# Kernel tuning notes

Measured on AMD Instinct MI355X. Metric: run time of the kernel, lower is better.

The kernel has to match this reference:

```python
import jax, jax.numpy as jnp
import numpy as np

EPS = 1e-12  # torch F.normalize eps

def _l2norm(t, axis):
    n = jnp.linalg.norm(t, axis=axis, keepdims=True)
    return t / jnp.maximum(n, EPS)

def setup_inputs() -> dict:
    key = jax.random.key(0)
    ks = jax.random.split(key, 7)
    B, L, D, F, K = 16, 128, 512, 1024, 16
    return {
        "x": jax.random.normal(ks[0], (B, L, D), jnp.float32),
        "W_gate_basis": jax.random.normal(ks[1], (K, D, F), jnp.float32) * (1.0 / np.sqrt(D)),
        "W_up_basis": jax.random.normal(ks[2], (K, D, F), jnp.float32) * (1.0 / np.sqrt(D)),
        "W_down_basis": jax.random.normal(ks[3], (K, F, D), jnp.float32) * (1.0 / np.sqrt(F)),
        "token_coef1": jax.random.normal(ks[4], (L, K), jnp.float32),
        "token_coef2": jax.random.normal(ks[5], (L, K), jnp.float32),
        "token_coef3": jax.random.normal(ks[6], (L, K), jnp.float32),
        "u_scale_param": jnp.ones((1, F), jnp.float32),
        "v_scale_param": jnp.ones((1, F), jnp.float32),
    }

def reference(x, W_gate_basis, W_up_basis, W_down_basis,
              token_coef1, token_coef2, token_coef3,
              u_scale_param, v_scale_param):
    D = x.shape[-1]
    c1 = jax.nn.softmax(token_coef1, axis=-1)
    c2 = jax.nn.softmax(token_coef2, axis=-1)
    c3 = jax.nn.softmax(token_coef3, axis=-1)
    # per-token weights [L, D, F] / [L, F, D]
    W_gate = jnp.einsum('lk,kio->lio', c1, W_gate_basis)
    W_up = jnp.einsum('lk,kio->lio', c2, W_up_basis)
    W_down = jnp.einsum('lk,koj->loj', c3, W_down_basis)
    W_gate = _l2norm(W_gate, axis=1)   # normalize over input dim D
    W_up = _l2norm(W_up, axis=1)
    W_down = _l2norm(W_down, axis=1)   # normalize over hidden dim F
    u = jnp.einsum('bld,ldf->blf', x, W_gate)
    v = jnp.einsum('bld,ldf->blf', x, W_up)
    u_scale = jnp.abs(u_scale_param) * 1.0
    v_scale = jnp.abs(v_scale_param) * jnp.sqrt(jnp.float32(D))
    h = jax.nn.silu(v_scale * v) * (u_scale * u)
    out = jnp.einsum('blf,lfd->bld', h, W_down)
    return _l2norm(out, axis=-1)
```

## Files before the change

kernel.cpp:

```cpp
#include <hip/hip_runtime.h>
#include <hip/hip_bf16.h>
#include <cmath>


typedef _Float16 half8 __attribute__((ext_vector_type(8)));
typedef _Float16 half4 __attribute__((ext_vector_type(4)));
typedef float    f32x4 __attribute__((ext_vector_type(4)));
typedef float    f32x2 __attribute__((ext_vector_type(2)));

#define MFMA_F16  __builtin_amdgcn_mfma_f32_16x16x32_f16
#define MFMA16    __builtin_amdgcn_mfma_f32_16x16x16f16

#define LDS_BARRIER()                                           \
    do {                                                        \
        asm volatile("s_waitcnt lgkmcnt(0)" ::: "memory");      \
        __builtin_amdgcn_s_barrier();                           \
    } while (0)

static constexpr size_t OFF_P1  = 0;
static constexpr size_t OFF_P2  = 16777216;
static constexpr size_t OFF_P3n = 17825792;
static constexpr size_t OFF_XA  = 33554432;
static constexpr size_t OFF_U2  = 35651584;
static constexpr size_t OFF_S   = 39845888;
// ... 22 lines not shown
#pragma unroll
    for (int k = 0; k < 16; ++k) {
        f32x4 v = *(const f32x4*)(
            src + (size_t)k * Amin * Bmaj + (size_t)(m0 + row) * Bmaj + M0 + cg * 4);
        f32x2 lo = { v[0], v[1] };
        f32x2 hi = { v[2], v[3] };
        *(f32x2*)(&S[k * 1088 + row * 34 + cg * 4])     = lo;
        *(f32x2*)(&S[k * 1088 + row * 34 + cg * 4 + 2]) = hi;
    }
    __syncthreads();

    int mn = t & 31, mjq = t >> 5;
#pragma unroll
    for (int q = 0; q < 4; ++q) {
        int mj = q * 8 + mjq;
        half8 v0, v1;
#pragma unroll
        for (int k = 0; k < 8; ++k) v0[k] = (_Float16)S[k * 1088 + mn * 34 + mj];
#pragma unroll
        for (int k = 0; k < 8; ++k) v1[k] = (_Float16)S[(k + 8) * 1088 + mn * 34 + mj];
        _Float16* out = dst + ((size_t)(M0 + mj) * Amin + m0 + mn) * 16;
        *(half8*)out       = v0;
        *(half8*)(out + 8) = v1;
    }
}

__global__ __launch_bounds__(256) void prep_x(
    const float* __restrict__ x, _Float16* __restrict__ XA)
{
    int l = blockIdx.x >> 1, bh = blockIdx.x & 1;
    __shared__ __align__(16) _Float16 XT[8][524];
    int t = threadIdx.x;

    int bl = t >> 5, q = t & 31;
    int b = bh * 8 + bl;
#pragma unroll
    for (int j = 0; j < 4; ++j) {
        f32x4 v = *(const f32x4*)(x + ((size_t)(b * 128 + l) * 512 + j * 128 + q * 4));
#pragma unroll
        for (int i = 0; i < 4; ++i)
            XT[bl][j * 128 + q * 4 + i] = (_Float16)v[i];
    }
    __syncthreads();

    int c = t >> 2, bi = t & 3;
#pragma unroll
    for (int s = 0; s < 2; ++s) {
        int blw = bi * 2 + s;
        half8 h = *(const half8*)(&XT[blw][c * 8]);
        *(half8*)(XA + (((size_t)(l * 64 + c) * 16 + bh * 8 + blw) * 8)) = h;
    }
}

__global__ __launch_bounds__(256, 4) void up_split(
    const _Float16* __restrict__ P1, const _Float16* __restrict__ P2,
    const _Float16* __restrict__ XA,
    const float* __restrict__ tc1, const float* __restrict__ tc2,
    const float* __restrict__ usp, const float* __restrict__ vsp,
    _Float16* __restrict__ U2, _Float16* __restrict__ S)
{
    int bid = blockIdx.x;
    int mh = bid >> 9;
    int lg = (bid >> 6) & 7;
    int f0 = (bid & 63) * 16;
    int tid = threadIdx.x;
    int w = tid >> 6, lane = tid & 63;
    int n = lane & 15, kc = lane >> 4;

    const _Float16* P  = mh ? P2 : P1;
    const float*    tc = mh ? tc2 : tc1;

    __shared__ __align__(16) _Float16 Wt[2][16 * 584];
    __shared__ float CN[256];

    const _Float16* pP  = P + ((size_t)(f0 + w * 4) * 512 + n) * 16 + kc * 4;
    const _Float16* pXA = XA + (((size_t)(lg * 16 + w * 4) * 64 + kc) * 16 + n) * 8;

    half4 pa[4][2];
#pragma unroll
    for (int fl = 0; fl < 4; ++fl)
#pragma unroll
        for (int dg = 0; dg < 2; ++dg)
            pa[fl][dg] = *(const half4*)(pP + fl * 8192 + dg * 256);
    const _Float16* qP = pP + 512;

    if (tid < 16) {
        const float* row = tc + (size_t)(lg * 16 + tid) * 16;
        float e[16], m = -1e30f, sum = 0.f;
#pragma unroll
        for (int k = 0; k < 16; ++k) m = fmaxf(m, row[k]);
#pragma unroll
        for (int k = 0; k < 16; ++k) { e[k] = __expf(row[k] - m); sum += e[k]; }
        float r = 1.f / sum;
#pragma unroll
        for (int k = 0; k < 16; ++k) CN[tid * 16 + k] = e[k] * r;
    }
    __syncthreads();

    half4 cf;
#pragma unroll
    for (int j = 0; j < 4; ++j)
        cf[j] = (_Float16)CN[n * 16 + kc * 4 + j];

    f32x4 zf = { 0.f, 0.f, 0.f, 0.f };
    f32x4 aU[4];
#pragma unroll
    for (int i = 0; i < 4; ++i) aU[i] = zf;
    float nsq[4] = { 0.f, 0.f, 0.f, 0.f };
    half8 xf[4];

#pragma unroll 1
    for (int it = 0; it < 16; ++it) {
        _Float16* WtW = &Wt[it & 1][0];
        const _Float16* WtR = &Wt[(it & 1) ^ 1][0];

#pragma unroll
        for (int fl = 0; fl < 4; ++fl) {
            int f_l = w * 4 + fl;
#pragma unroll
            for (int dg = 0; dg < 2; ++dg) {
                f32x4 c1 = MFMA16(pa[fl][dg], cf, zf, 0, 0, 0);
                nsq[fl] += c1[0] * c1[0] + c1[1] * c1[1]
                         + c1[2] * c1[2] + c1[3] * c1[3];
                half4 h1 = { (_Float16)c1[0], (_Float16)c1[1],
                             (_Float16)c1[2], (_Float16)c1[3] };
                *(half4*)(&WtW[n * 584 + f_l * 36 + dg * 16 + kc * 4]) = h1;
            }
        }
        if (it < 15) {
#pragma unroll
            for (int fl = 0; fl < 4; ++fl)
#pragma unroll
                for (int dg = 0; dg < 2; ++dg)
                    pa[fl][dg] = *(const half4*)(qP + fl * 8192 + dg * 256);
        }
        if (it > 0) {
#pragma unroll
            for (int li = 0; li < 4; ++li) {
                int l = w * 4 + li;
                half8 wU = *(const half8*)(&WtR[l * 584 + n * 36 + kc * 8]);
                aU[li] = MFMA_F16(xf[li], wU, aU[li], 0, 0, 0);
            }
        }
#pragma unroll
        for (int li = 0; li < 4; ++li)
            xf[li] = *(const half8*)(pXA + li * 8192);
        pXA += 512;
        qP += 512;
        LDS_BARRIER();
    }
#pragma unroll
    for (int li = 0; li < 4; ++li) {
        int l = w * 4 + li;
        half8 wU = *(const half8*)(&Wt[1][l * 584 + n * 36 + kc * 8]);
        aU[li] = MFMA_F16(xf[li], wU, aU[li], 0, 0, 0);
    }

#pragma unroll
    for (int fl = 0; fl < 4; ++fl) {
        float vU = nsq[fl];
        vU += __shfl_xor(vU, 16); vU += __shfl_xor(vU, 32);
        if (kc == 0) CN[n * 16 + w * 4 + fl] = vU;
    }
    __syncthreads();

    int f = f0 + n;
    float sc = mh ? (fabsf(vsp[f]) * 22.627416997969522f)
                  : fabsf(usp[f]);
    _Float16* Out = mh ? S : U2;
#pragma unroll
    for (int li = 0; li < 4; ++li) {
        int lgl = lg * 16 + w * 4 + li;
        float r1 = 1.f / fmaxf(sqrtf(CN[(w * 4 + li) * 16 + n]), 1e-12f);
#pragma unroll
        for (int i = 0; i < 4; ++i) {
            float val = aU[li][i] * r1 * sc;
            if (mh) val = val / (1.f + __expf(-val));
            Out[(((size_t)lgl * 128 + (f >> 3)) * 16 + kc * 4 + i) * 8 + (f & 7)] =
                (_Float16)val;
        }
    }
}

__global__ __launch_bounds__(256, 4) void down_fast(
    const _Float16* __restrict__ P3, const float* __restrict__ tc3,
    const _Float16* __restrict__ S, const _Float16* __restrict__ U2,
    float* __restrict__ Rp, float* __restrict__ Np)
{
    int zh = blockIdx.x >> 8;
    int rem = blockIdx.x & 255;
    int lg = rem >> 5;
    int d0 = (rem & 31) * 16;
    int tid = threadIdx.x;
    int w = tid >> 6, lane = tid & 63;
    int n = lane & 15, kc = lane >> 4;

    __shared__ __align__(16) _Float16 Wt[2][16 * 584];
    __shared__ float CN[256];

    const _Float16* pP3 = P3 + ((size_t)(d0 + w * 4) * 1024 + zh * 256 + n) * 16 + kc * 4;
    size_t hoff = (((size_t)(lg * 16 + w * 4) * 128 + zh * 32 + kc) * 16 + n) * 8;
    const _Float16* pS = S + hoff;
    const _Float16* pU = U2 + hoff;

    half4 pa[4][2];
#pragma unroll
    for (int dl = 0; dl < 4; ++dl)
#pragma unroll
        for (int fg = 0; fg < 2; ++fg)
            pa[dl][fg] = *(const half4*)(pP3 + dl * 16384 + fg * 256);
    const _Float16* qP3 = pP3 + 512;

    if (tid < 16) {
        const float* row = tc3 + (size_t)(lg * 16 + tid) * 16;
        float e[16], m = -1e30f, sum = 0.f;
#pragma unroll
        for (int k = 0; k < 16; ++k) m = fmaxf(m, row[k]);
#pragma unroll
        for (int k = 0; k < 16; ++k) { e[k] = __expf(row[k] - m); sum += e[k]; }
        float r = 1.f / sum;
#pragma unroll
        for (int k = 0; k < 16; ++k) CN[tid * 16 + k] = e[k] * r;
    }
    __syncthreads();

    half4 cf3;
#pragma unroll
    for (int j = 0; j < 4; ++j)
        cf3[j] = (_Float16)CN[n * 16 + kc * 4 + j];

    f32x4 zf = { 0.f, 0.f, 0.f, 0.f };
    f32x4 aO[4];
#pragma unroll
    for (int i = 0; i < 4; ++i) aO[i] = zf;
    float nsqD[4] = { 0.f, 0.f, 0.f, 0.f };
    half8 hf[4];

#pragma unroll 1
    for (int it = 0; it < 8; ++it) {
        _Float16* WtW = &Wt[it & 1][0];
        const _Float16* WtR = &Wt[(it & 1) ^ 1][0];

#pragma unroll
        for (int dl = 0; dl < 4; ++dl) {
            int d_l = w * 4 + dl;
#pragma unroll
            for (int fg = 0; fg < 2; ++fg) {
                f32x4 cw = MFMA16(pa[dl][fg], cf3, zf, 0, 0, 0);
                nsqD[dl] += cw[0] * cw[0] + cw[1] * cw[1]
                          + cw[2] * cw[2] + cw[3] * cw[3];
                half4 h4 = { (_Float16)cw[0], (_Float16)cw[1],
                             (_Float16)cw[2], (_Float16)cw[3] };
                *(half4*)(&WtW[n * 584 + d_l * 36 + fg * 16 + kc * 4]) = h4;
            }
        }
        if (it < 7) {
#pragma unroll
            for (int dl = 0; dl < 4; ++dl)
#pragma unroll
                for (int fg = 0; fg < 2; ++fg)
                    pa[dl][fg] = *(const half4*)(qP3 + dl * 16384 + fg * 256);
        }
        if (it > 0) {
#pragma unroll
            for (int li = 0; li < 4; ++li) {
                int l = w * 4 + li;
                half8 wf = *(const half8*)(&WtR[l * 584 + n * 36 + kc * 8]);
                aO[li] = MFMA_F16(hf[li], wf, aO[li], 0, 0, 0);
            }
        }
#pragma unroll
        for (int li = 0; li < 4; ++li) {
            half8 s8 = *(const half8*)(pS + li * 16384);
            half8 u8 = *(const half8*)(pU + li * 16384);
            hf[li] = s8 * u8;
        }
        pS += 512;
        pU += 512;
        qP3 += 512;
        LDS_BARRIER();
    }
#pragma unroll
    for (int li = 0; li < 4; ++li) {
        int l = w * 4 + li;
        half8 wf = *(const half8*)(&Wt[1][l * 584 + n * 36 + kc * 8]);
        aO[li] = MFMA_F16(hf[li], wf, aO[li], 0, 0, 0);
    }

#pragma unroll
    for (int dl = 0; dl < 4; ++dl) {
        float v = nsqD[dl];
        v += __shfl_xor(v, 16); v += __shfl_xor(v, 32);
        if (kc == 0)
            Np[(size_t)zh * 65536 + (size_t)(lg * 16 + n) * 512 + d0 + w * 4 + dl] = v;
    }
#pragma unroll
    for (int li = 0; li < 4; ++li) {
        int lgl = lg * 16 + w * 4 + li;
#pragma unroll
        for (int i = 0; i < 4; ++i)
            Rp[(size_t)zh * 1048576 +
               ((size_t)(kc * 4 + i) * 128 + lgl) * 512 + d0 + n] = aO[li][i];
    }
}

__global__ __launch_bounds__(128) void final_combine(
    const float* __restrict__ Rp, const float* __restrict__ Np,
    float* __restrict__ out)
{
    int rid = blockIdx.x;
    int l = rid & 127;
    int t = threadIdx.x;
    f32x4 r = { 0.f, 0.f, 0.f, 0.f };
    f32x4 nn = { 0.f, 0.f, 0.f, 0.f };
#pragma unroll
    for (int zh = 0; zh < 4; ++zh) {
        f32x4 rz = *(const f32x4*)(Rp + (size_t)zh * 1048576 + (size_t)rid * 512 + t * 4);
        f32x4 nz = *(const f32x4*)(Np + (size_t)zh * 65536 + (size_t)l * 512 + t * 4);
#pragma unroll
        for (int j = 0; j < 4; ++j) { r[j] += rz[j]; nn[j] += nz[j]; }
    }
    f32x4 y;
#pragma unroll
    for (int j = 0; j < 4; ++j) {
        float rr = 1.f / fmaxf(sqrtf(fmaxf(nn[j], 0.f)), 1e-12f);
        y[j] = r[j] * rr;
    }
    float s = y[0] * y[0] + y[1] * y[1] + y[2] * y[2] + y[3] * y[3];
#pragma unroll
    for (int off = 32; off > 0; off >>= 1) s += __shfl_down(s, off);
    __shared__ float sred[2];
    if ((t & 63) == 0) sred[t >> 6] = s;
    __syncthreads();
    float rr = 1.f / fmaxf(sqrtf(sred[0] + sred[1]), 1e-12f);
    f32x4 o = { y[0] * rr, y[1] * rr, y[2] * rr, y[3] * rr };
    *(f32x4*)(out + (size_t)rid * 512 + t * 4) = o;
}

__global__ __launch_bounds__(256) void up_kernel(
    const float* __restrict__ x,
    const float* __restrict__ wg, const float* __restrict__ wu,
    const float* __restrict__ tc1, const float* __restrict__ tc2,
    const float* __restrict__ usp, const float* __restrict__ vsp,
    _Float16* __restrict__ Hp)
{
    int lg = blockIdx.x >> 6;
    int f0 = (blockIdx.x & 63) * 16;
    int tid = threadIdx.x;
    int w = tid >> 6, lane = tid & 63;
    int n = lane & 15, kc = lane >> 4;

    __shared__ __align__(16) _Float16 Xt[256 * 40];
    __shared__ __align__(16) _Float16 Bh[32 * 16 * 24];
    __shared__ __align__(16) _Float16 Wt[16 * 528];
    __shared__ float CN[2 * 16 * 16];
// ... 250 lines not shown
        int lgl = lg * 16 + w * 4 + li;
        float r3 = 1.f / fmaxf(sqrtf(CN[(w * 4 + li) * 16 + n]), 1e-12f);
#pragma unroll
        for (int i = 0; i < 4; ++i)
            out[((size_t)(kc * 4 + i) * 128 + lgl) * 512 + d0 + n] = aO[li][i] * r3;
    }
}

__global__ __launch_bounds__(128) void final_kernel(float* __restrict__ out)
{
    int rid = blockIdx.x;
    int t = threadIdx.x;
    f32x4 y = *(const f32x4*)(out + (size_t)rid * 512 + t * 4);
    float s = y[0] * y[0] + y[1] * y[1] + y[2] * y[2] + y[3] * y[3];
#pragma unroll
    for (int off = 32; off > 0; off >>= 1) s += __shfl_down(s, off);
    __shared__ float sred[2];
    if ((t & 63) == 0) sred[t >> 6] = s;
    __syncthreads();
    float rr = 1.f / fmaxf(sqrtf(sred[0] + sred[1]), 1e-12f);
    f32x4 o = { y[0] * rr, y[1] * rr, y[2] * rr, y[3] * rr };
    *(f32x4*)(out + (size_t)rid * 512 + t * 4) = o;
}

extern "C" void kernel_launch(void* const* d_in, const int* in_sizes, int n_in,
                              void* d_out, int out_size, void* d_ws, size_t ws_size,
                              hipStream_t stream)
{
    (void)in_sizes; (void)n_in; (void)out_size;
    const float* x   = (const float*)d_in[0];
    const float* wg  = (const float*)d_in[1];
    const float* wu  = (const float*)d_in[2];
    const float* wd  = (const float*)d_in[3];
    const float* tc1 = (const float*)d_in[4];
    const float* tc2 = (const float*)d_in[5];
    const float* tc3 = (const float*)d_in[6];
    const float* usp = (const float*)d_in[7];
    const float* vsp = (const float*)d_in[8];
    float* outp = (float*)d_out;
    char* ws = (char*)d_ws;

    if (ws_size >= WS_FAST) {
        _Float16* P1  = (_Float16*)(ws + OFF_P1);
        _Float16* P2  = (_Float16*)(ws + OFF_P2);
        _Float16* P3n = (_Float16*)(ws + OFF_P3n);
        _Float16* XA  = (_Float16*)(ws + OFF_XA);
        _Float16* U2  = (_Float16*)(ws + OFF_U2);
        _Float16* S   = (_Float16*)(ws + OFF_S);
        float* Rp = (float*)(ws + OFF_P1);
        float* Np = (float*)(ws + OFF_P2);
        prep_basis_all<<<dim3(512, 2), dim3(256), 0, stream>>>(
            wg, wu, wd, P1, P2, P3n, 0);
        prep_x<<<dim3(256), dim3(256), 0, stream>>>(x, XA);
        up_split<<<dim3(1024), dim3(256), 0, stream>>>(P1, P2, XA, tc1, tc2,
                                                       usp, vsp, U2, S);
        prep_basis_all<<<dim3(512, 1), dim3(256), 0, stream>>>(
            wg, wu, wd, P1, P2, P3n, 2);
        down_fast<<<dim3(1024), dim3(256), 0, stream>>>(P3n, tc3, S, U2, Rp, Np);
        final_combine<<<dim3(2048), dim3(128), 0, stream>>>(Rp, Np, outp);
    } else {
        _Float16* Hp = (_Float16*)ws;
        up_kernel<<<dim3(512), dim3(256), 0, stream>>>(x, wg, wu, tc1, tc2,
                                                       usp, vsp, Hp);
        down_kernel<<<dim3(256), dim3(256), 0, stream>>>(wd, tc3, Hp, outp);
        final_kernel<<<dim3(2048), dim3(128), 0, stream>>>(outp);
    }
}
```

Before: 227.1 us.

## Unroll main loops by two with even/odd register sets for deeper prefetch

```diff
diff --git a/kernel.cpp b/kernel.cpp
--- a/kernel.cpp
+++ b/kernel.cpp
@@ -118,17 +118,26 @@
 
     __shared__ __align__(16) _Float16 Wt[2][16 * 584];
     __shared__ float CN[256];
+    _Float16* Wt0 = &Wt[0][0];
+    _Float16* Wt1 = &Wt[1][0];
 
     const _Float16* pP  = P + ((size_t)(f0 + w * 4) * 512 + n) * 16 + kc * 4;
     const _Float16* pXA = XA + (((size_t)(lg * 16 + w * 4) * 64 + kc) * 16 + n) * 8;
 
-    half4 pa[4][2];
+    half4 paE[4][2], paO[4][2];
+    half8 xfE[4], xfO[4];
 #pragma unroll
     for (int fl = 0; fl < 4; ++fl)
 #pragma unroll
-        for (int dg = 0; dg < 2; ++dg)
-            pa[fl][dg] = *(const half4*)(pP + fl * 8192 + dg * 256);
-    const _Float16* qP = pP + 512;
+        for (int dg = 0; dg < 2; ++dg) {
+            paE[fl][dg] = *(const half4*)(pP + fl * 8192 + dg * 256);
+            paO[fl][dg] = *(const half4*)(pP + 512 + fl * 8192 + dg * 256);
+        }
+#pragma unroll
+    for (int li = 0; li < 4; ++li)
+        xfE[li] = *(const half8*)(pXA + li * 8192);
+    const _Float16* qP  = pP + 1024;
+    const _Float16* qXA = pXA + 512;
 
     if (tid < 16) {
         const float* row = tc + (size_t)(lg * 16 + tid) * 16;
@@ -153,53 +162,120 @@
 #pragma unroll
     for (int i = 0; i < 4; ++i) aU[i] = zf;
     float nsq[4] = { 0.f, 0.f, 0.f, 0.f };
-    half8 xf[4];
 
 #pragma unroll 1
-    for (int it = 0; it < 16; ++it) {
-        _Float16* WtW = &Wt[it & 1][0];
-        const _Float16* WtR = &Wt[(it & 1) ^ 1][0];
-
+    for (int it2 = 0; it2 < 7; ++it2) {
 #pragma unroll
         for (int fl = 0; fl < 4; ++fl) {
             int f_l = w * 4 + fl;
 #pragma unroll
             for (int dg = 0; dg < 2; ++dg) {
-                f32x4 c1 = MFMA16(pa[fl][dg], cf, zf, 0, 0, 0);
+                f32x4 c1 = MFMA16(paE[fl][dg], cf, zf, 0, 0, 0);
                 nsq[fl] += c1[0] * c1[0] + c1[1] * c1[1]
                          + c1[2] * c1[2] + c1[3] * c1[3];
                 half4 h1 = { (_Float16)c1[0], (_Float16)c1[1],
                              (_Float16)c1[2], (_Float16)c1[3] };
-                *(half4*)(&WtW[n * 584 + f_l * 36 + dg * 16 + kc * 4]) = h1;
+                *(half4*)(&Wt0[n * 584 + f_l * 36 + dg * 16 + kc * 4]) = h1;
             }
         }
-        if (it < 15) {
-#pragma unroll
-            for (int fl = 0; fl < 4; ++fl)
-#pragma unroll
-                for (int dg = 0; dg < 2; ++dg)
-                    pa[fl][dg] = *(const half4*)(qP + fl * 8192 + dg * 256);
-        }
-        if (it > 0) {
+#pragma unroll
+        for (int fl = 0; fl < 4; ++fl)
+#pragma unroll
+            for (int dg = 0; dg < 2; ++dg)
+                paE[fl][dg] = *(const half4*)(qP + fl * 8192 + dg * 256);
+        qP += 512;
+        if (it2 > 0) {
 #pragma unroll
             for (int li = 0; li < 4; ++li) {
                 int l = w * 4 + li;
-                half8 wU = *(const half8*)(&WtR[l * 584 + n * 36 + kc * 8]);
-                aU[li] = MFMA_F16(xf[li], wU, aU[li], 0, 0, 0);
+                half8 wU = *(const half8*)(&Wt1[l * 584 + n * 36 + kc * 8]);
+                aU[li] = MFMA_F16(xfO[li], wU, aU[li], 0, 0, 0);
             }
         }
 #pragma unroll
         for (int li = 0; li < 4; ++li)
-            xf[li] = *(const half8*)(pXA + li * 8192);
-        pXA += 512;
+            xfO[li] = *(const half8*)(qXA + li * 8192);
+        qXA += 512;
+        LDS_BARRIER();
+#pragma unroll
+        for (int fl = 0; fl < 4; ++fl) {
+            int f_l = w * 4 + fl;
+#pragma unroll
+            for (int dg = 0; dg < 2; ++dg) {
+                f32x4 c1 = MFMA16(paO[fl][dg], cf, zf, 0, 0, 0);
+                nsq[fl] += c1[0] * c1[0] + c1[1] * c1[1]
+                         + c1[2] * c1[2] + c1[3] * c1[3];
+                half4 h1 = { (_Float16)c1[0], (_Float16)c1[1],
+                             (_Float16)c1[2], (_Float16)c1[3] };
+                *(half4*)(&Wt1[n * 584 + f_l * 36 + dg * 16 + kc * 4]) = h1;
+            }
+        }
+#pragma unroll
+        for (int fl = 0; fl < 4; ++fl)
+#pragma unroll
+            for (int dg = 0; dg < 2; ++dg)
+                paO[fl][dg] = *(const half4*)(qP + fl * 8192 + dg * 256);
         qP += 512;
+#pragma unroll
+        for (int li = 0; li < 4; ++li) {
+            int l = w * 4 + li;
+            half8 wU = *(const half8*)(&Wt0[l * 584 + n * 36 + kc * 8]);
+            aU[li] = MFMA_F16(xfE[li], wU, aU[li], 0, 0, 0);
+        }
+#pragma unroll
+        for (int li = 0; li < 4; ++li)
+            xfE[li] = *(const half8*)(qXA + li * 8192);
+        qXA += 512;
         LDS_BARRIER();
     }
 #pragma unroll
+    for (int fl = 0; fl < 4; ++fl) {
+        int f_l = w * 4 + fl;
+#pragma unroll
+        for (int dg = 0; dg < 2; ++dg) {
+            f32x4 c1 = MFMA16(paE[fl][dg], cf, zf, 0, 0, 0);
+            nsq[fl] += c1[0] * c1[0] + c1[1] * c1[1]
+                     + c1[2] * c1[2] + c1[3] * c1[3];
+            half4 h1 = { (_Float16)c1[0], (_Float16)c1[1],
+                         (_Float16)c1[2], (_Float16)c1[3] };
+            *(half4*)(&Wt0[n * 584 + f_l * 36 + dg * 16 + kc * 4]) = h1;
+        }
+    }
+#pragma unroll
     for (int li = 0; li < 4; ++li) {
         int l = w * 4 + li;
-        half8 wU = *(const half8*)(&Wt[1][l * 584 + n * 36 + kc * 8]);
-        aU[li] = MFMA_F16(xf[li], wU, aU[li], 0, 0, 0);
+        half8 wU = *(const half8*)(&Wt1[l * 584 + n * 36 + kc * 8]);
+        aU[li] = MFMA_F16(xfO[li], wU, aU[li], 0, 0, 0);
+    }
+#pragma unroll
+    for (int li = 0; li < 4; ++li)
+        xfO[li] = *(const half8*)(qXA + li * 8192);
+    LDS_BARRIER();
+#pragma unroll
+    for (int fl = 0; fl < 4; ++fl) {
+        int f_l = w * 4 + fl;
+#pragma unroll
+        for (int dg = 0; dg < 2; ++dg) {
+            f32x4 c1 = MFMA16(paO[fl][dg], cf, zf, 0, 0, 0);
+            nsq[fl] += c1[0] * c1[0] + c1[1] * c1[1]
+                     + c1[2] * c1[2] + c1[3] * c1[3];
+            half4 h1 = { (_Float16)c1[0], (_Float16)c1[1],
+                         (_Float16)c1[2], (_Float16)c1[3] };
+            *(half4*)(&Wt1[n * 584 + f_l * 36 + dg * 16 + kc * 4]) = h1;
+        }
+    }
+#pragma unroll
+    for (int li = 0; li < 4; ++li) {
+        int l = w * 4 + li;
+        half8 wU = *(const half8*)(&Wt0[l * 584 + n * 36 + kc * 8]);
+        aU[li] = MFMA_F16(xfE[li], wU, aU[li], 0, 0, 0);
+    }
+    LDS_BARRIER();
+#pragma unroll
+    for (int li = 0; li < 4; ++li) {
+        int l = w * 4 + li;
+        half8 wU = *(const half8*)(&Wt1[l * 584 + n * 36 + kc * 8]);
+        aU[li] = MFMA_F16(xfO[li], wU, aU[li], 0, 0, 0);
     }
 
 #pragma unroll
@@ -243,19 +319,23 @@
 
     __shared__ __align__(16) _Float16 Wt[2][16 * 584];
     __shared__ float CN[256];
+    _Float16* Wt0 = &Wt[0][0];
+    _Float16* Wt1 = &Wt[1][0];
 
     const _Float16* pP3 = P3 + ((size_t)(d0 + w * 4) * 1024 + zh * 256 + n) * 16 + kc * 4;
     size_t hoff = (((size_t)(lg * 16 + w * 4) * 128 + zh * 32 + kc) * 16 + n) * 8;
     const _Float16* pS = S + hoff;
     const _Float16* pU = U2 + hoff;
 
-    half4 pa[4][2];
+    half4 paE[4][2], paO[4][2];
 #pragma unroll
     for (int dl = 0; dl < 4; ++dl)
 #pragma unroll
-        for (int fg = 0; fg < 2; ++fg)
-            pa[dl][fg] = *(const half4*)(pP3 + dl * 16384 + fg * 256);
-    const _Float16* qP3 = pP3 + 512;
+        for (int fg = 0; fg < 2; ++fg) {
+            paE[dl][fg] = *(const half4*)(pP3 + dl * 16384 + fg * 256);
+            paO[dl][fg] = *(const half4*)(pP3 + 512 + dl * 16384 + fg * 256);
+        }
+    const _Float16* qP3 = pP3 + 1024;
 
     if (tid < 16) {
         const float* row = tc3 + (size_t)(lg * 16 + tid) * 16;
@@ -283,35 +363,31 @@
     half8 hf[4];
 
 #pragma unroll 1
-    for (int it = 0; it < 8; ++it) {
-        _Float16* WtW = &Wt[it & 1][0];
-        const _Float16* WtR = &Wt[(it & 1) ^ 1][0];
-
+    for (int it2 = 0; it2 < 3; ++it2) {
 #pragma unroll
         for (int dl = 0; dl < 4; ++dl) {
             int d_l = w * 4 + dl;
 #pragma unroll
             for (int fg = 0; fg < 2; ++fg) {
-                f32x4 cw = MFMA16(pa[dl][fg], cf3, zf, 0, 0, 0);
+                f32x4 cw = MFMA16(paE[dl][fg], cf3, zf, 0, 0, 0);
                 nsqD[dl] += cw[0] * cw[0] + cw[1] * cw[1]
                           + cw[2] * cw[2] + cw[3] * cw[3];
                 half4 h4 = { (_Float16)cw[0], (_Float16)cw[1],
                              (_Float16)cw[2], (_Float16)cw[3] };
-                *(half4*)(&WtW[n * 584 + d_l * 36 + fg * 16 + kc * 4]) = h4;
+                *(half4*)(&Wt0[n * 584 + d_l * 36 + fg * 16 + kc * 4]) = h4;
             }
         }
-        if (it < 7) {
-#pragma unroll
-            for (int dl = 0; dl < 4; ++dl)
-#pragma unroll
-                for (int fg = 0; fg < 2; ++fg)
-                    pa[dl][fg] = *(const half4*)(qP3 + dl * 16384 + fg * 256);
-        }
-        if (it > 0) {
+#pragma unroll
+        for (int dl = 0; dl < 4; ++dl)
+#pragma unroll
+            for (int fg = 0; fg < 2; ++fg)
+                paE[dl][fg] = *(const half4*)(qP3 + dl * 16384 + fg * 256);
+        qP3 += 512;
+        if (it2 > 0) {
 #pragma unroll
             for (int li = 0; li < 4; ++li) {
                 int l = w * 4 + li;
-                half8 wf = *(const half8*)(&WtR[l * 584 + n * 36 + kc * 8]);
+                half8 wf = *(const half8*)(&Wt1[l * 584 + n * 36 + kc * 8]);
                 aO[li] = MFMA_F16(hf[li], wf, aO[li], 0, 0, 0);
             }
         }
@@ -323,13 +399,100 @@
         }
         pS += 512;
         pU += 512;
+        LDS_BARRIER();
+#pragma unroll
+        for (int dl = 0; dl < 4; ++dl) {
+            int d_l = w * 4 + dl;
+#pragma unroll
+            for (int fg = 0; fg < 2; ++fg) {
+                f32x4 cw = MFMA16(paO[dl][fg], cf3, zf, 0, 0, 0);
+                nsqD[dl] += cw[0] * cw[0] + cw[1] * cw[1]
+                          + cw[2] * cw[2] + cw[3] * cw[3];
+                half4 h4 = { (_Float16)cw[0], (_Float16)cw[1],
+                             (_Float16)cw[2], (_Float16)cw[3] };
+                *(half4*)(&Wt1[n * 584 + d_l * 36 + fg * 16 + kc * 4]) = h4;
+            }
+        }
+#pragma unroll
+        for (int dl = 0; dl < 4; ++dl)
+#pragma unroll
+            for (int fg = 0; fg < 2; ++fg)
+                paO[dl][fg] = *(const half4*)(qP3 + dl * 16384 + fg * 256);
         qP3 += 512;
+#pragma unroll
+        for (int li = 0; li < 4; ++li) {
+            int l = w * 4 + li;
+            half8 wf = *(const half8*)(&Wt0[l * 584 + n * 36 + kc * 8]);
+            aO[li] = MFMA_F16(hf[li], wf, aO[li], 0, 0, 0);
+        }
+#pragma unroll
+        for (int li = 0; li < 4; ++li) {
+            half8 s8 = *(const half8*)(pS + li * 16384);
+            half8 u8 = *(const half8*)(pU + li * 16384);
+            hf[li] = s8 * u8;
+        }
+        pS += 512;
+        pU += 512;
         LDS_BARRIER();
     }
 #pragma unroll
+    for (int dl = 0; dl < 4; ++dl) {
+        int d_l = w * 4 + dl;
+#pragma unroll
+        for (int fg = 0; fg < 2; ++fg) {
+            f32x4 cw = MFMA16(paE[dl][fg], cf3, zf, 0, 0, 0);
+            nsqD[dl] += cw[0] * cw[0] + cw[1] * cw[1]
+                      + cw[2] * cw[2] + cw[3] * cw[3];
+            half4 h4 = { (_Float16)cw[0], (_Float16)cw[1],
+                         (_Float16)cw[2], (_Float16)cw[3] };
+            *(half4*)(&Wt0[n * 584 + d_l * 36 + fg * 16 + kc * 4]) = h4;
+        }
+    }
+#pragma unroll
     for (int li = 0; li < 4; ++li) {
         int l = w * 4 + li;
-        half8 wf = *(const half8*)(&Wt[1][l * 584 + n * 36 + kc * 8]);
+        half8 wf = *(const half8*)(&Wt1[l * 584 + n * 36 + kc * 8]);
+        aO[li] = MFMA_F16(hf[li], wf, aO[li], 0, 0, 0);
+    }
+#pragma unroll
+    for (int li = 0; li < 4; ++li) {
+        half8 s8 = *(const half8*)(pS + li * 16384);
+        half8 u8 = *(const half8*)(pU + li * 16384);
+        hf[li] = s8 * u8;
+    }
+    pS += 512;
+    pU += 512;
+    LDS_BARRIER();
+#pragma unroll
+    for (int dl = 0; dl < 4; ++dl) {
+        int d_l = w * 4 + dl;
+#pragma unroll
+        for (int fg = 0; fg < 2; ++fg) {
+            f32x4 cw = MFMA16(paO[dl][fg], cf3, zf, 0, 0, 0);
+            nsqD[dl] += cw[0] * cw[0] + cw[1] * cw[1]
+                      + cw[2] * cw[2] + cw[3] * cw[3];
+            half4 h4 = { (_Float16)cw[0], (_Float16)cw[1],
+                         (_Float16)cw[2], (_Float16)cw[3] };
+            *(half4*)(&Wt1[n * 584 + d_l * 36 + fg * 16 + kc * 4]) = h4;
+        }
+    }
+#pragma unroll
+    for (int li = 0; li < 4; ++li) {
+        int l = w * 4 + li;
+        half8 wf = *(const half8*)(&Wt0[l * 584 + n * 36 + kc * 8]);
+        aO[li] = MFMA_F16(hf[li], wf, aO[li], 0, 0, 0);
+    }
+#pragma unroll
+    for (int li = 0; li < 4; ++li) {
+        half8 s8 = *(const half8*)(pS + li * 16384);
+        half8 u8 = *(const half8*)(pU + li * 16384);
+        hf[li] = s8 * u8;
+    }
+    LDS_BARRIER();
+#pragma unroll
+    for (int li = 0; li < 4; ++li) {
+        int l = w * 4 + li;
+        half8 wf = *(const half8*)(&Wt1[l * 584 + n * 36 + kc * 8]);
         aO[li] = MFMA_F16(hf[li], wf, aO[li], 0, 0, 0);
     }
 
```

After: 247.0 us. 1.09x slower.

## Double tile width in up and down kernels so x/h fragments are reused

Applied to the files above, without the earlier changes.

```diff
diff --git a/kernel.cpp b/kernel.cpp
--- a/kernel.cpp
+++ b/kernel.cpp
@@ -98,7 +98,7 @@
     }
 }
 
-__global__ __launch_bounds__(256, 4) void up_split(
+__global__ __launch_bounds__(512, 2) void up_split(
     const _Float16* __restrict__ P1, const _Float16* __restrict__ P2,
     const _Float16* __restrict__ XA,
     const float* __restrict__ tc1, const float* __restrict__ tc2,
@@ -106,21 +106,26 @@
     _Float16* __restrict__ U2, _Float16* __restrict__ S)
 {
     int bid = blockIdx.x;
-    int mh = bid >> 9;
-    int lg = (bid >> 6) & 7;
-    int f0 = (bid & 63) * 16;
+    int mh = bid >> 8;
+    int lg = (bid >> 5) & 7;
+    int f0 = (bid & 31) * 32;
     int tid = threadIdx.x;
-    int w = tid >> 6, lane = tid & 63;
+    int wq = tid >> 6;
+    int lane = tid & 63;
     int n = lane & 15, kc = lane >> 4;
+    int lh = wq & 3;
+    int fh = wq >> 2;
 
     const _Float16* P  = mh ? P2 : P1;
     const float*    tc = mh ? tc2 : tc1;
 
-    __shared__ __align__(16) _Float16 Wt[2][16 * 584];
-    __shared__ float CN[256];
-
-    const _Float16* pP  = P + ((size_t)(f0 + w * 4) * 512 + n) * 16 + kc * 4;
-    const _Float16* pXA = XA + (((size_t)(lg * 16 + w * 4) * 64 + kc) * 16 + n) * 8;
+    __shared__ __align__(16) _Float16 Wt[2][16 * 1168];
+    __shared__ float CN[512];
+    _Float16* Wt0 = &Wt[0][0];
+    _Float16* Wt1 = &Wt[1][0];
+
+    const _Float16* pP  = P + ((size_t)(f0 + wq * 4) * 512 + n) * 16 + kc * 4;
+    const _Float16* pXA = XA + (((size_t)(lg * 16 + lh * 4) * 64 + kc) * 16 + n) * 8;
 
     half4 pa[4][2];
 #pragma unroll
@@ -147,6 +152,7 @@
 #pragma unroll
     for (int j = 0; j < 4; ++j)
         cf[j] = (_Float16)CN[n * 16 + kc * 4 + j];
+    __syncthreads();
 
     f32x4 zf = { 0.f, 0.f, 0.f, 0.f };
     f32x4 aU[4];
@@ -157,12 +163,12 @@
 
 #pragma unroll 1
     for (int it = 0; it < 16; ++it) {
-        _Float16* WtW = &Wt[it & 1][0];
-        const _Float16* WtR = &Wt[(it & 1) ^ 1][0];
+        _Float16* WtW = (it & 1) ? Wt1 : Wt0;
+        const _Float16* WtR = (it & 1) ? Wt0 : Wt1;
 
 #pragma unroll
         for (int fl = 0; fl < 4; ++fl) {
-            int f_l = w * 4 + fl;
+            int f_l = wq * 4 + fl;
 #pragma unroll
             for (int dg = 0; dg < 2; ++dg) {
                 f32x4 c1 = MFMA16(pa[fl][dg], cf, zf, 0, 0, 0);
@@ -170,7 +176,7 @@
                          + c1[2] * c1[2] + c1[3] * c1[3];
                 half4 h1 = { (_Float16)c1[0], (_Float16)c1[1],
                              (_Float16)c1[2], (_Float16)c1[3] };
-                *(half4*)(&WtW[n * 584 + f_l * 36 + dg * 16 + kc * 4]) = h1;
+                *(half4*)(&WtW[n * 1168 + f_l * 36 + dg * 16 + kc * 4]) = h1;
             }
         }
         if (it < 15) {
@@ -183,8 +189,9 @@
         if (it > 0) {
 #pragma unroll
             for (int li = 0; li < 4; ++li) {
-                int l = w * 4 + li;
-                half8 wU = *(const half8*)(&WtR[l * 584 + n * 36 + kc * 8]);
+                int l = lh * 4 + li;
+                half8 wU = *(const half8*)(
+                    &WtR[l * 1168 + (fh * 16 + n) * 36 + kc * 8]);
                 aU[li] = MFMA_F16(xf[li], wU, aU[li], 0, 0, 0);
             }
         }
@@ -197,8 +204,9 @@
     }
 #pragma unroll
     for (int li = 0; li < 4; ++li) {
-        int l = w * 4 + li;
-        half8 wU = *(const half8*)(&Wt[1][l * 584 + n * 36 + kc * 8]);
+        int l = lh * 4 + li;
+        half8 wU = *(const half8*)(
+            &Wt1[l * 1168 + (fh * 16 + n) * 36 + kc * 8]);
         aU[li] = MFMA_F16(xf[li], wU, aU[li], 0, 0, 0);
     }
 
@@ -206,18 +214,19 @@
     for (int fl = 0; fl < 4; ++fl) {
         float vU = nsq[fl];
         vU += __shfl_xor(vU, 16); vU += __shfl_xor(vU, 32);
-        if (kc == 0) CN[n * 16 + w * 4 + fl] = vU;
-    }
-    __syncthreads();
-
-    int f = f0 + n;
+        if (kc == 0) CN[n * 32 + wq * 4 + fl] = vU;
+    }
+    __syncthreads();
+
+    int f = f0 + fh * 16 + n;
     float sc = mh ? (fabsf(vsp[f]) * 22.627416997969522f)
                   : fabsf(usp[f]);
     _Float16* Out = mh ? S : U2;
 #pragma unroll
     for (int li = 0; li < 4; ++li) {
-        int lgl = lg * 16 + w * 4 + li;
-        float r1 = 1.f / fmaxf(sqrtf(CN[(w * 4 + li) * 16 + n]), 1e-12f);
+        int ll = lh * 4 + li;
+        int lgl = lg * 16 + ll;
+        float r1 = 1.f / fmaxf(sqrtf(CN[ll * 32 + fh * 16 + n]), 1e-12f);
 #pragma unroll
         for (int i = 0; i < 4; ++i) {
             float val = aU[li][i] * r1 * sc;
@@ -228,24 +237,29 @@
     }
 }
 
-__global__ __launch_bounds__(256, 4) void down_fast(
+__global__ __launch_bounds__(512, 2) void down_fast(
     const _Float16* __restrict__ P3, const float* __restrict__ tc3,
     const _Float16* __restrict__ S, const _Float16* __restrict__ U2,
     float* __restrict__ Rp, float* __restrict__ Np)
 {
-    int zh = blockIdx.x >> 8;
-    int rem = blockIdx.x & 255;
-    int lg = rem >> 5;
-    int d0 = (rem & 31) * 16;
+    int bid = blockIdx.x;
+    int zh = bid >> 7;
+    int lg = (bid >> 4) & 7;
+    int d0 = (bid & 15) * 32;
     int tid = threadIdx.x;
-    int w = tid >> 6, lane = tid & 63;
+    int wq = tid >> 6;
+    int lane = tid & 63;
     int n = lane & 15, kc = lane >> 4;
-
-    __shared__ __align__(16) _Float16 Wt[2][16 * 584];
-    __shared__ float CN[256];
-
-    const _Float16* pP3 = P3 + ((size_t)(d0 + w * 4) * 1024 + zh * 256 + n) * 16 + kc * 4;
-    size_t hoff = (((size_t)(lg * 16 + w * 4) * 128 + zh * 32 + kc) * 16 + n) * 8;
+    int lh = wq & 3;
+    int dh = wq >> 2;
+
+    __shared__ __align__(16) _Float16 Wt[2][16 * 1168];
+    __shared__ float CN[512];
+    _Float16* Wt0 = &Wt[0][0];
+    _Float16* Wt1 = &Wt[1][0];
+
+    const _Float16* pP3 = P3 + ((size_t)(d0 + wq * 4) * 1024 + zh * 256 + n) * 16 + kc * 4;
+    size_t hoff = (((size_t)(lg * 16 + lh * 4) * 128 + zh * 32 + kc) * 16 + n) * 8;
     const _Float16* pS = S + hoff;
     const _Float16* pU = U2 + hoff;
 
@@ -274,6 +288,7 @@
 #pragma unroll
     for (int j = 0; j < 4; ++j)
         cf3[j] = (_Float16)CN[n * 16 + kc * 4 + j];
+    __syncthreads();
 
     f32x4 zf = { 0.f, 0.f, 0.f, 0.f };
     f32x4 aO[4];
@@ -284,12 +299,12 @@
 
 #pragma unroll 1
     for (int it = 0; it < 8; ++it) {
-        _Float16* WtW = &Wt[it & 1][0];
-        const _Float16* WtR = &Wt[(it & 1) ^ 1][0];
+        _Float16* WtW = (it & 1) ? Wt1 : Wt0;
+        const _Float16* WtR = (it & 1) ? Wt0 : Wt1;
 
 #pragma unroll
         for (int dl = 0; dl < 4; ++dl) {
-            int d_l = w * 4 + dl;
+            int d_l = wq * 4 + dl;
 #pragma unroll
             for (int fg = 0; fg < 2; ++fg) {
                 f32x4 cw = MFMA16(pa[dl][fg], cf3, zf, 0, 0, 0);
@@ -297,7 +312,7 @@
                           + cw[2] * cw[2] + cw[3] * cw[3];
                 half4 h4 = { (_Float16)cw[0], (_Float16)cw[1],
                              (_Float16)cw[2], (_Float16)cw[3] };
-                *(half4*)(&WtW[n * 584 + d_l * 36 + fg * 16 + kc * 4]) = h4;
+                *(half4*)(&WtW[n * 1168 + d_l * 36 + fg * 16 + kc * 4]) = h4;
             }
         }
         if (it < 7) {
@@ -310,8 +325,9 @@
         if (it > 0) {
 #pragma unroll
             for (int li = 0; li < 4; ++li) {
-                int l = w * 4 + li;
-                half8 wf = *(const half8*)(&WtR[l * 584 + n * 36 + kc * 8]);
+                int l = lh * 4 + li;
+                half8 wf = *(const half8*)(
+                    &WtR[l * 1168 + (dh * 16 + n) * 36 + kc * 8]);
                 aO[li] = MFMA_F16(hf[li], wf, aO[li], 0, 0, 0);
             }
         }
@@ -328,8 +344,9 @@
     }
 #pragma unroll
     for (int li = 0; li < 4; ++li) {
-        int l = w * 4 + li;
-        half8 wf = *(const half8*)(&Wt[1][l * 584 + n * 36 + kc * 8]);
+        int l = lh * 4 + li;
+        half8 wf = *(const half8*)(
+            &Wt1[l * 1168 + (dh * 16 + n) * 36 + kc * 8]);
         aO[li] = MFMA_F16(hf[li], wf, aO[li], 0, 0, 0);
     }
 
@@ -338,15 +355,15 @@
         float v = nsqD[dl];
         v += __shfl_xor(v, 16); v += __shfl_xor(v, 32);
         if (kc == 0)
-            Np[(size_t)zh * 65536 + (size_t)(lg * 16 + n) * 512 + d0 + w * 4 + dl] = v;
+            Np[(size_t)zh * 65536 + (size_t)(lg * 16 + n) * 512 + d0 + wq * 4 + dl] = v;
     }
 #pragma unroll
     for (int li = 0; li < 4; ++li) {
-        int lgl = lg * 16 + w * 4 + li;
+        int lgl = lg * 16 + lh * 4 + li;
 #pragma unroll
         for (int i = 0; i < 4; ++i)
             Rp[(size_t)zh * 1048576 +
-               ((size_t)(kc * 4 + i) * 128 + lgl) * 512 + d0 + n] = aO[li][i];
+               ((size_t)(kc * 4 + i) * 128 + lgl) * 512 + d0 + dh * 16 + n] = aO[li][i];
     }
 }
 
@@ -703,11 +720,11 @@
         prep_basis_all<<<dim3(512, 2), dim3(256), 0, stream>>>(
             wg, wu, wd, P1, P2, P3n, 0);
         prep_x<<<dim3(256), dim3(256), 0, stream>>>(x, XA);
-        up_split<<<dim3(1024), dim3(256), 0, stream>>>(P1, P2, XA, tc1, tc2,
-                                                       usp, vsp, U2, S);
+        up_split<<<dim3(512), dim3(512), 0, stream>>>(P1, P2, XA, tc1, tc2,
+                                                      usp, vsp, U2, S);
         prep_basis_all<<<dim3(512, 1), dim3(256), 0, stream>>>(
             wg, wu, wd, P1, P2, P3n, 2);
-        down_fast<<<dim3(1024), dim3(256), 0, stream>>>(P3n, tc3, S, U2, Rp, Np);
+        down_fast<<<dim3(512), dim3(512), 0, stream>>>(P3n, tc3, S, U2, Rp, Np);
         final_combine<<<dim3(2048), dim3(128), 0, stream>>>(Rp, Np, outp);
     } else {
         _Float16* Hp = (_Float16*)ws;
```

New measurement: 239.7 us. 1.06x slower.

## Process two token groups per block to reuse basis loads in up/down kernels

Applied to the files above, without the earlier changes.

```diff
diff --git a/kernel.cpp b/kernel.cpp
--- a/kernel.cpp
+++ b/kernel.cpp
@@ -98,7 +98,7 @@
     }
 }
 
-__global__ __launch_bounds__(256, 4) void up_split(
+__global__ __launch_bounds__(256, 2) void up_split(
     const _Float16* __restrict__ P1, const _Float16* __restrict__ P2,
     const _Float16* __restrict__ XA,
     const float* __restrict__ tc1, const float* __restrict__ tc2,
@@ -106,8 +106,8 @@
     _Float16* __restrict__ U2, _Float16* __restrict__ S)
 {
     int bid = blockIdx.x;
-    int mh = bid >> 9;
-    int lg = (bid >> 6) & 7;
+    int mh = bid >> 8;
+    int lgp = (bid >> 6) & 3;
     int f0 = (bid & 63) * 16;
     int tid = threadIdx.x;
     int w = tid >> 6, lane = tid & 63;
@@ -116,11 +116,12 @@
     const _Float16* P  = mh ? P2 : P1;
     const float*    tc = mh ? tc2 : tc1;
 
-    __shared__ __align__(16) _Float16 Wt[2][16 * 584];
-    __shared__ float CN[256];
+    __shared__ __align__(16) _Float16 Wt[2][2][16 * 584];
+    __shared__ float CN[512];
 
     const _Float16* pP  = P + ((size_t)(f0 + w * 4) * 512 + n) * 16 + kc * 4;
-    const _Float16* pXA = XA + (((size_t)(lg * 16 + w * 4) * 64 + kc) * 16 + n) * 8;
+    const _Float16* pXA = XA +
+        (((size_t)(lgp * 32 + w * 4) * 64 + kc) * 16 + n) * 8;
 
     half4 pa[4][2];
 #pragma unroll
@@ -130,8 +131,8 @@
             pa[fl][dg] = *(const half4*)(pP + fl * 8192 + dg * 256);
     const _Float16* qP = pP + 512;
 
-    if (tid < 16) {
-        const float* row = tc + (size_t)(lg * 16 + tid) * 16;
+    if (tid < 32) {
+        const float* row = tc + (size_t)(lgp * 32 + tid) * 16;
         float e[16], m = -1e30f, sum = 0.f;
 #pragma unroll
         for (int k = 0; k < 16; ++k) m = fmaxf(m, row[k]);
@@ -143,34 +144,46 @@
     }
     __syncthreads();
 
-    half4 cf;
-#pragma unroll
-    for (int j = 0; j < 4; ++j)
-        cf[j] = (_Float16)CN[n * 16 + kc * 4 + j];
+    half4 cf0, cf1;
+#pragma unroll
+    for (int j = 0; j < 4; ++j) {
+        cf0[j] = (_Float16)CN[n * 16 + kc * 4 + j];
+        cf1[j] = (_Float16)CN[(16 + n) * 16 + kc * 4 + j];
+    }
+    __syncthreads();
 
     f32x4 zf = { 0.f, 0.f, 0.f, 0.f };
-    f32x4 aU[4];
-#pragma unroll
-    for (int i = 0; i < 4; ++i) aU[i] = zf;
-    float nsq[4] = { 0.f, 0.f, 0.f, 0.f };
-    half8 xf[4];
+    f32x4 aU0[4], aU1[4];
+#pragma unroll
+    for (int i = 0; i < 4; ++i) { aU0[i] = zf; aU1[i] = zf; }
+    float nsq0[4] = { 0.f, 0.f, 0.f, 0.f };
+    float nsq1[4] = { 0.f, 0.f, 0.f, 0.f };
+    half8 xf0[4], xf1[4];
 
 #pragma unroll 1
     for (int it = 0; it < 16; ++it) {
-        _Float16* WtW = &Wt[it & 1][0];
-        const _Float16* WtR = &Wt[(it & 1) ^ 1][0];
+        _Float16* W0 = &Wt[it & 1][0][0];
+        _Float16* W1 = &Wt[it & 1][1][0];
+        const _Float16* R0 = &Wt[(it & 1) ^ 1][0][0];
+        const _Float16* R1 = &Wt[(it & 1) ^ 1][1][0];
 
 #pragma unroll
         for (int fl = 0; fl < 4; ++fl) {
             int f_l = w * 4 + fl;
 #pragma unroll
             for (int dg = 0; dg < 2; ++dg) {
-                f32x4 c1 = MFMA16(pa[fl][dg], cf, zf, 0, 0, 0);
-                nsq[fl] += c1[0] * c1[0] + c1[1] * c1[1]
-                         + c1[2] * c1[2] + c1[3] * c1[3];
+                f32x4 c0 = MFMA16(pa[fl][dg], cf0, zf, 0, 0, 0);
+                nsq0[fl] += c0[0] * c0[0] + c0[1] * c0[1]
+                          + c0[2] * c0[2] + c0[3] * c0[3];
+                half4 h0 = { (_Float16)c0[0], (_Float16)c0[1],
+                             (_Float16)c0[2], (_Float16)c0[3] };
+                *(half4*)(&W0[n * 584 + f_l * 36 + dg * 16 + kc * 4]) = h0;
+                f32x4 c1 = MFMA16(pa[fl][dg], cf1, zf, 0, 0, 0);
+                nsq1[fl] += c1[0] * c1[0] + c1[1] * c1[1]
+                          + c1[2] * c1[2] + c1[3] * c1[3];
                 half4 h1 = { (_Float16)c1[0], (_Float16)c1[1],
                              (_Float16)c1[2], (_Float16)c1[3] };
-                *(half4*)(&WtW[n * 584 + f_l * 36 + dg * 16 + kc * 4]) = h1;
+                *(half4*)(&W1[n * 584 + f_l * 36 + dg * 16 + kc * 4]) = h1;
             }
         }
         if (it < 15) {
@@ -184,13 +197,17 @@
 #pragma unroll
             for (int li = 0; li < 4; ++li) {
                 int l = w * 4 + li;
-                half8 wU = *(const half8*)(&WtR[l * 584 + n * 36 + kc * 8]);
-                aU[li] = MFMA_F16(xf[li], wU, aU[li], 0, 0, 0);
+                half8 w0 = *(const half8*)(&R0[l * 584 + n * 36 + kc * 8]);
+                half8 w1 = *(const half8*)(&R1[l * 584 + n * 36 + kc * 8]);
+                aU0[li] = MFMA_F16(xf0[li], w0, aU0[li], 0, 0, 0);
+                aU1[li] = MFMA_F16(xf1[li], w1, aU1[li], 0, 0, 0);
             }
         }
 #pragma unroll
-        for (int li = 0; li < 4; ++li)
-            xf[li] = *(const half8*)(pXA + li * 8192);
+        for (int li = 0; li < 4; ++li) {
+            xf0[li] = *(const half8*)(pXA + li * 8192);
+            xf1[li] = *(const half8*)(pXA + 131072 + li * 8192);
+        }
         pXA += 512;
         qP += 512;
         LDS_BARRIER();
@@ -198,15 +215,21 @@
 #pragma unroll
     for (int li = 0; li < 4; ++li) {
         int l = w * 4 + li;
-        half8 wU = *(const half8*)(&Wt[1][l * 584 + n * 36 + kc * 8]);
-        aU[li] = MFMA_F16(xf[li], wU, aU[li], 0, 0, 0);
+        half8 w0 = *(const half8*)(&Wt[1][0][l * 584 + n * 36 + kc * 8]);
+        half8 w1 = *(const half8*)(&Wt[1][1][l * 584 + n * 36 + kc * 8]);
+        aU0[li] = MFMA_F16(xf0[li], w0, aU0[li], 0, 0, 0);
+        aU1[li] = MFMA_F16(xf1[li], w1, aU1[li], 0, 0, 0);
     }
 
 #pragma unroll
     for (int fl = 0; fl < 4; ++fl) {
-        float vU = nsq[fl];
-        vU += __shfl_xor(vU, 16); vU += __shfl_xor(vU, 32);
-        if (kc == 0) CN[n * 16 + w * 4 + fl] = vU;
+        float v0 = nsq0[fl], v1 = nsq1[fl];
+        v0 += __shfl_xor(v0, 16); v0 += __shfl_xor(v0, 32);
+        v1 += __shfl_xor(v1, 16); v1 += __shfl_xor(v1, 32);
+        if (kc == 0) {
+            CN[0 * 256 + n * 16 + w * 4 + fl] = v0;
+            CN[1 * 256 + n * 16 + w * 4 + fl] = v1;
+        }
     }
     __syncthreads();
 
@@ -216,36 +239,44 @@
     _Float16* Out = mh ? S : U2;
 #pragma unroll
     for (int li = 0; li < 4; ++li) {
-        int lgl = lg * 16 + w * 4 + li;
-        float r1 = 1.f / fmaxf(sqrtf(CN[(w * 4 + li) * 16 + n]), 1e-12f);
+        int lgl0 = lgp * 32 + w * 4 + li;
+        int lgl1 = lgl0 + 16;
+        float r0 = 1.f / fmaxf(sqrtf(CN[0 * 256 + (w * 4 + li) * 16 + n]), 1e-12f);
+        float r1 = 1.f / fmaxf(sqrtf(CN[1 * 256 + (w * 4 + li) * 16 + n]), 1e-12f);
 #pragma unroll
         for (int i = 0; i < 4; ++i) {
-            float val = aU[li][i] * r1 * sc;
-            if (mh) val = val / (1.f + __expf(-val));
-            Out[(((size_t)lgl * 128 + (f >> 3)) * 16 + kc * 4 + i) * 8 + (f & 7)] =
-                (_Float16)val;
-        }
-    }
-}
-
-__global__ __launch_bounds__(256, 4) void down_fast(
+            float v0 = aU0[li][i] * r0 * sc;
+            float v1 = aU1[li][i] * r1 * sc;
+            if (mh) {
+                v0 = v0 / (1.f + __expf(-v0));
+                v1 = v1 / (1.f + __expf(-v1));
+            }
+            Out[(((size_t)lgl0 * 128 + (f >> 3)) * 16 + kc * 4 + i) * 8 + (f & 7)] =
+                (_Float16)v0;
+            Out[(((size_t)lgl1 * 128 + (f >> 3)) * 16 + kc * 4 + i) * 8 + (f & 7)] =
+                (_Float16)v1;
+        }
+    }
+}
+
+__global__ __launch_bounds__(256, 2) void down_fast(
     const _Float16* __restrict__ P3, const float* __restrict__ tc3,
     const _Float16* __restrict__ S, const _Float16* __restrict__ U2,
     float* __restrict__ Rp, float* __restrict__ Np)
 {
-    int zh = blockIdx.x >> 8;
-    int rem = blockIdx.x & 255;
-    int lg = rem >> 5;
-    int d0 = (rem & 31) * 16;
+    int bid = blockIdx.x;
+    int zh = bid >> 7;
+    int lgp = (bid >> 5) & 3;
+    int d0 = (bid & 31) * 16;
     int tid = threadIdx.x;
     int w = tid >> 6, lane = tid & 63;
     int n = lane & 15, kc = lane >> 4;
 
-    __shared__ __align__(16) _Float16 Wt[2][16 * 584];
-    __shared__ float CN[256];
+    __shared__ __align__(16) _Float16 Wt[2][2][16 * 584];
+    __shared__ float CN[512];
 
     const _Float16* pP3 = P3 + ((size_t)(d0 + w * 4) * 1024 + zh * 256 + n) * 16 + kc * 4;
-    size_t hoff = (((size_t)(lg * 16 + w * 4) * 128 + zh * 32 + kc) * 16 + n) * 8;
+    size_t hoff = (((size_t)(lgp * 32 + w * 4) * 128 + zh * 32 + kc) * 16 + n) * 8;
     const _Float16* pS = S + hoff;
     const _Float16* pU = U2 + hoff;
 
@@ -257,8 +288,8 @@
             pa[dl][fg] = *(const half4*)(pP3 + dl * 16384 + fg * 256);
     const _Float16* qP3 = pP3 + 512;
 
-    if (tid < 16) {
-        const float* row = tc3 + (size_t)(lg * 16 + tid) * 16;
+    if (tid < 32) {
+        const float* row = tc3 + (size_t)(lgp * 32 + tid) * 16;
         float e[16], m = -1e30f, sum = 0.f;
 #pragma unroll
         for (int k = 0; k < 16; ++k) m = fmaxf(m, row[k]);
@@ -270,34 +301,46 @@
     }
     __syncthreads();
 
-    half4 cf3;
-#pragma unroll
-    for (int j = 0; j < 4; ++j)
-        cf3[j] = (_Float16)CN[n * 16 + kc * 4 + j];
+    half4 cf30, cf31;
+#pragma unroll
+    for (int j = 0; j < 4; ++j) {
+        cf30[j] = (_Float16)CN[n * 16 + kc * 4 + j];
+        cf31[j] = (_Float16)CN[(16 + n) * 16 + kc * 4 + j];
+    }
+    __syncthreads();
 
     f32x4 zf = { 0.f, 0.f, 0.f, 0.f };
-    f32x4 aO[4];
-#pragma unroll
-    for (int i = 0; i < 4; ++i) aO[i] = zf;
-    float nsqD[4] = { 0.f, 0.f, 0.f, 0.f };
-    half8 hf[4];
+    f32x4 aO0[4], aO1[4];
+#pragma unroll
+    for (int i = 0; i < 4; ++i) { aO0[i] = zf; aO1[i] = zf; }
+    float nsq0[4] = { 0.f, 0.f, 0.f, 0.f };
+    float nsq1[4] = { 0.f, 0.f, 0.f, 0.f };
+    half8 hf0[4], hf1[4];
 
 #pragma unroll 1
     for (int it = 0; it < 8; ++it) {
-        _Float16* WtW = &Wt[it & 1][0];
-        const _Float16* WtR = &Wt[(it & 1) ^ 1][0];
+        _Float16* W0 = &Wt[it & 1][0][0];
+        _Float16* W1 = &Wt[it & 1][1][0];
+        const _Float16* R0 = &Wt[(it & 1) ^ 1][0][0];
+        const _Float16* R1 = &Wt[(it & 1) ^ 1][1][0];
 
 #pragma unroll
         for (int dl = 0; dl < 4; ++dl) {
             int d_l = w * 4 + dl;
 #pragma unroll
             for (int fg = 0; fg < 2; ++fg) {
-                f32x4 cw = MFMA16(pa[dl][fg], cf3, zf, 0, 0, 0);
-                nsqD[dl] += cw[0] * cw[0] + cw[1] * cw[1]
-                          + cw[2] * cw[2] + cw[3] * cw[3];
-                half4 h4 = { (_Float16)cw[0], (_Float16)cw[1],
-                             (_Float16)cw[2], (_Float16)cw[3] };
-                *(half4*)(&WtW[n * 584 + d_l * 36 + fg * 16 + kc * 4]) = h4;
+                f32x4 c0 = MFMA16(pa[dl][fg], cf30, zf, 0, 0, 0);
+                nsq0[dl] += c0[0] * c0[0] + c0[1] * c0[1]
+                          + c0[2] * c0[2] + c0[3] * c0[3];
+                half4 h0 = { (_Float16)c0[0], (_Float16)c0[1],
+                             (_Float16)c0[2], (_Float16)c0[3] };
+                *(half4*)(&W0[n * 584 + d_l * 36 + fg * 16 + kc * 4]) = h0;
+                f32x4 c1 = MFMA16(pa[dl][fg], cf31, zf, 0, 0, 0);
+                nsq1[dl] += c1[0] * c1[0] + c1[1] * c1[1]
+                          + c1[2] * c1[2] + c1[3] * c1[3];
+                half4 h1 = { (_Float16)c1[0], (_Float16)c1[1],
+                             (_Float16)c1[2], (_Float16)c1[3] };
+                *(half4*)(&W1[n * 584 + d_l * 36 + fg * 16 + kc * 4]) = h1;
             }
         }
         if (it < 7) {
@@ -311,15 +354,20 @@
 #pragma unroll
             for (int li = 0; li < 4; ++li) {
                 int l = w * 4 + li;
-                half8 wf = *(const half8*)(&WtR[l * 584 + n * 36 + kc * 8]);
-                aO[li] = MFMA_F16(hf[li], wf, aO[li], 0, 0, 0);
+                half8 w0 = *(const half8*)(&R0[l * 584 + n * 36 + kc * 8]);
+                half8 w1 = *(const half8*)(&R1[l * 584 + n * 36 + kc * 8]);
+                aO0[li] = MFMA_F16(hf0[li], w0, aO0[li], 0, 0, 0);
+                aO1[li] = MFMA_F16(hf1[li], w1, aO1[li], 0, 0, 0);
             }
         }
 #pragma unroll
         for (int li = 0; li < 4; ++li) {
-            half8 s8 = *(const half8*)(pS + li * 16384);
-            half8 u8 = *(const half8*)(pU + li * 16384);
-            hf[li] = s8 * u8;
+            half8 s0 = *(const half8*)(pS + li * 16384);
+            half8 u0 = *(const half8*)(pU + li * 16384);
+            hf0[li] = s0 * u0;
+            half8 s1 = *(const half8*)(pS + 262144 + li * 16384);
+            half8 u1 = *(const half8*)(pU + 262144 + li * 16384);
+            hf1[li] = s1 * u1;
         }
         pS += 512;
         pU += 512;
@@ -329,24 +377,33 @@
 #pragma unroll
     for (int li = 0; li < 4; ++li) {
         int l = w * 4 + li;
-        half8 wf = *(const half8*)(&Wt[1][l * 584 + n * 36 + kc * 8]);
-        aO[li] = MFMA_F16(hf[li], wf, aO[li], 0, 0, 0);
+        half8 w0 = *(const half8*)(&Wt[1][0][l * 584 + n * 36 + kc * 8]);
+        half8 w1 = *(const half8*)(&Wt[1][1][l * 584 + n * 36 + kc * 8]);
+        aO0[li] = MFMA_F16(hf0[li], w0, aO0[li], 0, 0, 0);
+        aO1[li] = MFMA_F16(hf1[li], w1, aO1[li], 0, 0, 0);
     }
 
 #pragma unroll
     for (int dl = 0; dl < 4; ++dl) {
-        float v = nsqD[dl];
-        v += __shfl_xor(v, 16); v += __shfl_xor(v, 32);
-        if (kc == 0)
-            Np[(size_t)zh * 65536 + (size_t)(lg * 16 + n) * 512 + d0 + w * 4 + dl] = v;
+        float v0 = nsq0[dl], v1 = nsq1[dl];
+        v0 += __shfl_xor(v0, 16); v0 += __shfl_xor(v0, 32);
+        v1 += __shfl_xor(v1, 16); v1 += __shfl_xor(v1, 32);
+        if (kc == 0) {
+            Np[(size_t)zh * 65536 + (size_t)(lgp * 32 + n) * 512 + d0 + w * 4 + dl] = v0;
+            Np[(size_t)zh * 65536 + (size_t)(lgp * 32 + 16 + n) * 512 + d0 + w * 4 + dl] = v1;
+        }
     }
 #pragma unroll
     for (int li = 0; li < 4; ++li) {
-        int lgl = lg * 16 + w * 4 + li;
-#pragma unroll
-        for (int i = 0; i < 4; ++i)
+        int lgl0 = lgp * 32 + w * 4 + li;
+        int lgl1 = lgl0 + 16;
+#pragma unroll
+        for (int i = 0; i < 4; ++i) {
             Rp[(size_t)zh * 1048576 +
-               ((size_t)(kc * 4 + i) * 128 + lgl) * 512 + d0 + n] = aO[li][i];
+               ((size_t)(kc * 4 + i) * 128 + lgl0) * 512 + d0 + n] = aO0[li][i];
+            Rp[(size_t)zh * 1048576 +
+               ((size_t)(kc * 4 + i) * 128 + lgl1) * 512 + d0 + n] = aO1[li][i];
+        }
     }
 }
 
@@ -703,11 +760,11 @@
         prep_basis_all<<<dim3(512, 2), dim3(256), 0, stream>>>(
             wg, wu, wd, P1, P2, P3n, 0);
         prep_x<<<dim3(256), dim3(256), 0, stream>>>(x, XA);
-        up_split<<<dim3(1024), dim3(256), 0, stream>>>(P1, P2, XA, tc1, tc2,
-                                                       usp, vsp, U2, S);
+        up_split<<<dim3(512), dim3(256), 0, stream>>>(P1, P2, XA, tc1, tc2,
+                                                      usp, vsp, U2, S);
         prep_basis_all<<<dim3(512, 1), dim3(256), 0, stream>>>(
             wg, wu, wd, P1, P2, P3n, 2);
-        down_fast<<<dim3(1024), dim3(256), 0, stream>>>(P3n, tc3, S, U2, Rp, Np);
+        down_fast<<<dim3(512), dim3(256), 0, stream>>>(P3n, tc3, S, U2, Rp, Np);
         final_combine<<<dim3(2048), dim3(128), 0, stream>>>(Rp, Np, outp);
     } else {
         _Float16* Hp = (_Float16*)ws;
```

Result: no change. 228.7 us (+0.7%).
